# Kernel tuning notes

Measured on AMD Instinct MI355X. Metric: run time of the kernel, lower is better.

The kernel has to match this reference:

```python
import jax, jax.numpy as jnp
import numpy as np

EMB = 3          # embedding_size
NSIG = 1         # n_sigma
FG_W = 1.0       # foreground_weight
W_INST, W_VAR, W_SEED = 1.0, 10.0, 1.0
K_MAX = 8        # fixed number of instance ids (1..K_MAX); 0 is background


def _xyzm(T, H, W):
    # buffer is linspace over the FULL grid (32,800,2000), then sliced
    t = jnp.linspace(0.0, 0.1, 32)[:T]
    y = jnp.linspace(0.0, 1.6, 800)[:H]
    x = jnp.linspace(0.0, 4.16, 2000)[:W]
    tt = jnp.broadcast_to(t[:, None, None], (T, H, W))
    yy = jnp.broadcast_to(y[None, :, None], (T, H, W))
    xx = jnp.broadcast_to(x[None, None, :], (T, H, W))
    return jnp.stack([tt, yy, xx], 0)  # [3,T,H,W]


def _lovasz_hinge_flat(logits, labels):
    # standard Berman lovasz hinge on flat [N] logits/labels (labels in {0,1})
    signs = 2.0 * labels - 1.0
    errors = 1.0 - logits * signs
    order = jnp.argsort(-errors)             # descending errors
    errors_sorted = errors[order]
    gt_sorted = labels[order]
    gts = gt_sorted.sum()
    inter = gts - jnp.cumsum(gt_sorted)
    union = gts + jnp.cumsum(1.0 - gt_sorted)
    jac = 1.0 - inter / union
    grad = jnp.concatenate([jac[:1], jac[1:] - jac[:-1]])
    return jnp.dot(jax.nn.relu(errors_sorted), jax.lax.stop_gradient(grad))


def _forward(prediction, instances):
    B, C, T, H, W = prediction.shape
    xyzm = _xyzm(T, H, W).astype(prediction.dtype)

    emb = jnp.tanh(prediction[:, :EMB])                 # [B,3,T,H,W]
    spatial = emb + xyzm[None]                          # spatial_emb
    sigma = prediction[:, EMB]                          # [B,T,H,W] (n_sigma=1)
    seed = jax.nn.sigmoid(prediction[:, EMB + NSIG])    # [B,T,H,W]

    ids = jnp.arange(1, K_MAX + 1)
    masks = (instances[:, None] == ids[None, :, None, None, None]).astype(prediction.dtype)  # [B,K,T,H,W]
    counts = masks.sum((2, 3, 4))                       # [B,K]
    present = (counts > 0).astype(prediction.dtype)
    safe = jnp.maximum(counts, 1.0)

    # per-instance center of xyzm (to_center=True) and mean sigma
    centers = jnp.einsum('cthw,bkthw->bkc', xyzm, masks) / safe[..., None]   # [B,K,3]
    s_mean = jnp.einsum('bthw,bkthw->bk', sigma, masks) / safe               # [B,K]
    s_sg = jax.lax.stop_gradient(s_mean)

    # var loss: mean over mask of (sigma - stop_grad(s_mean))^2
    sig2 = jnp.einsum('bthw,bkthw->bk', sigma * sigma, masks) / safe
    var_k = sig2 - 2.0 * s_sg * s_mean + s_sg * s_sg                          # [B,K]

    # gaussian distance map: exp(-s * ||spatial - center||^2)
    s_exp = jnp.exp(s_mean * 10.0)                                            # [B,K]
    e2 = jnp.sum(spatial * spatial, axis=1)                                   # [B,T,H,W]
    ec = jnp.einsum('bcthw,bkc->bkthw', spatial, centers)                     # [B,K,T,H,W]
    c2 = jnp.sum(centers * centers, axis=-1)                                  # [B,K]
    sqdist = e2[:, None] - 2.0 * ec + c2[:, :, None, None, None]
    dist = jnp.exp(-s_exp[:, :, None, None, None] * sqdist)                   # [B,K,T,H,W]

    # lovasz hinge per instance
    logits = (dist * 2.0 - 1.0).reshape(B * K_MAX, -1)
    labels_flat = masks.reshape(B * K_MAX, -1)
    inst_k = jax.vmap(_lovasz_hinge_flat)(logits, labels_flat).reshape(B, K_MAX)

    obj = present.sum(1)
    safe_obj = jnp.maximum(obj, 1.0)
    inst_loss = (inst_k * present).sum(1) / safe_obj
    var_loss = (var_k * present).sum(1) / safe_obj

    # seed loss: background -> 0, foreground -> stop_grad(dist)
    bg = (instances == 0).astype(prediction.dtype)
    seed_bg = jnp.sum(bg * seed * seed, axis=(1, 2, 3))
    dsg = jax.lax.stop_gradient(dist)
    seed_fg = FG_W * jnp.sum(masks * (seed[:, None] - dsg) ** 2, axis=(1, 2, 3, 4))
    seed_loss = (seed_bg + seed_fg) / (H * W)

    return jnp.mean(W_INST * inst_loss + W_VAR * var_loss + W_SEED * seed_loss)


def setup_inputs() -> dict:
    key = jax.random.key(0)
    k1, k2, k3 = jax.random.split(key, 3)
    prediction = jax.random.normal(k1, (2, 5, 8, 256, 512), dtype=jnp.float32)
    instances = jax.random.randint(k2, (2, 8, 256, 512), 0, 9, dtype=jnp.int32)
    labels = jax.random.randint(k3, (2, 8, 256, 512), 0, 2, dtype=jnp.int32)
    return {"prediction": prediction, "instances": instances, "labels": labels}


def reference(prediction, instances, labels):
    # `labels` is accepted by the torch forward but unused in the loss math
    return _forward(prediction, instances)
```

## Files before the change

### kernel.cpp

```cpp
#include <hip/hip_runtime.h>
#include <math.h>

#define BB 2
#define KK 8
#define NB 256
#define HALF_NB_F 128.0f
#define FAR_CUT 5.5452f

#define PXB_H 1024
#define GRID_H 2048
#define PXB_A 4096
#define GRID_A 512
#define NPART_A 256

#define STEP_T (0.1f/31.0f)
#define STEP_Y (1.6f/799.0f)
#define STEP_X (4.16f/1999.0f)

#define OFF_ACC 0
#define OFF_PRM 100
#define OFF_GH2 512
#define OFF_PARTA 9216
#define OFF_SEED2 34816
#define OFF_HIST_F 40960

__global__ __launch_bounds__(256) void k_acc(const float* __restrict__ pred,
                                             const int* __restrict__ inst,
                                             float* __restrict__ ws) {
  int tid = threadIdx.x, blk = blockIdx.x;
  int b = blk >> 8;
  int rbase = (blk & 255) * PXB_A;
  const float* sig_p = pred + ((size_t)b * 5 << 20) + (3 << 20);
  const int* ip = inst + ((size_t)b << 20);
  float acc[48];
  #pragma unroll
  for (int f = 0; f < 48; ++f) acc[f] = 0.f;
  for (int it = 0; it < 4; ++it) {
    int r = rbase + it * 1024 + 4 * tid;
    float4 sg4 = *(const float4*)(sig_p + r);
    int4 id4 = *(const int4*)(ip + r);
    float tf = (float)(r >> 17), hf = (float)((r >> 9) & 255), wf = (float)(r & 511);
    float sv[4] = {sg4.x, sg4.y, sg4.z, sg4.w};
    int iv[4] = {id4.x, id4.y, id4.z, id4.w};
    #pragma unroll
    for (int j = 0; j < 4; ++j) {
      #pragma unroll
      for (int k = 0; k < KK; ++k) {
        float m = (iv[j] == k + 1) ? 1.f : 0.f;
        acc[k*6+0] += m;
        acc[k*6+1] += m * sv[j];
        acc[k*6+2] += m * sv[j] * sv[j];
        acc[k*6+3] += m * tf;
        acc[k*6+4] += m * hf;
        acc[k*6+5] += m * (wf + (float)j);
      }
    }
  }
  __shared__ float lds[4 * 48];
  int lane = tid & 63, wv = tid >> 6;
  #pragma unroll
  for (int f = 0; f < 48; ++f) {
    float v = acc[f];
    for (int o = 32; o; o >>= 1) v += __shfl_down(v, o);
    if (lane == 0) lds[wv * 48 + f] = v;
  }
  __syncthreads();
  if (tid < 48)
    ws[OFF_PARTA + ((size_t)b * 48 + tid) * NPART_A + (blk & 255)]
      = lds[tid] + lds[48 + tid] + lds[96 + tid] + lds[144 + tid];
}

__global__ __launch_bounds__(256) void k_params(float* __restrict__ ws) {
  __shared__ float accs[96];
  int tid = threadIdx.x;
  if (tid < 96) {
    const float* p = ws + OFF_PARTA + (size_t)tid * NPART_A;
    float s0 = 0.f, s1 = 0.f, s2 = 0.f, s3 = 0.f;
    for (int j = 0; j < NPART_A; j += 4) {
      s0 += p[j]; s1 += p[j+1]; s2 += p[j+2]; s3 += p[j+3];
    }
    accs[tid] = (s0 + s1) + (s2 + s3);
  }
  __syncthreads();
  if (tid < 16) {
    float* a = &accs[(tid >> 3) * 48 + (tid & 7) * 6];
    float cnt = a[0], s1 = a[1], s2 = a[2], st = a[3], sy = a[4], sx = a[5];
    float safe = fmaxf(cnt, 1.f);
    float smean = s1 / safe;
    ws[OFF_ACC + tid*6 + 0] = cnt;
    ws[OFF_PRM + tid*6 + 0] = st * STEP_T / safe;
    ws[OFF_PRM + tid*6 + 1] = sy * STEP_Y / safe;
    ws[OFF_PRM + tid*6 + 2] = sx * STEP_X / safe;
    ws[OFF_PRM + tid*6 + 3] = __expf(10.f * smean);
    ws[OFF_PRM + tid*6 + 4] = s2 / safe - smean * smean;
    ws[OFF_PRM + tid*6 + 5] = (cnt > 0.f) ? 1.f : 0.f;
  }
}

__device__ __forceinline__ float fast_tanh(float x) {
  x = fminf(fmaxf(x, -15.f), 15.f);
  float ex = __expf(2.f * x);
  return (ex - 1.f) / (ex + 1.f);
}

__global__ __launch_bounds__(256, 8) void k_hist(const float* __restrict__ pred,
                                                 const int* __restrict__ inst,
                                                 float* __restrict__ ws) {
  __shared__ unsigned int hist[KK * NB];
  __shared__ float Ps[KK * 4];
  __shared__ unsigned int pmask_s;
  __shared__ float wred[8];
  int tid = threadIdx.x;
  int blk = blockIdx.x;
  int b = blk >> 10;
  for (int i = tid; i < KK * NB; i += 256) hist[i] = 0u;
  if (tid < KK) {
    int seg = b * 8 + tid;
    Ps[tid*4+0] = ws[OFF_PRM + seg*6 + 0];
    Ps[tid*4+1] = ws[OFF_PRM + seg*6 + 1];
    Ps[tid*4+2] = ws[OFF_PRM + seg*6 + 2];
    Ps[tid*4+3] = ws[OFF_PRM + seg*6 + 3];
  }
  if (tid == 0) {
    unsigned m = 0;
    for (int k = 0; k < KK; ++k)
      if (ws[OFF_PRM + (b*8+k)*6 + 5] > 0.f) m |= 1u << k;
    pmask_s = m;
  }
  __syncthreads();
  unsigned pmask = pmask_s;
  int r = (blk & 1023) * PXB_H + 4 * tid;
  const float* pb = pred + ((size_t)b * 5 << 20);
  float tf = (float)(r >> 17), hf = (float)((r >> 9) & 255);
  int w = r & 511;
  float4 p0 = *(const float4*)(pb + r);
  float4 p1 = *(const float4*)(pb + (1 << 20) + r);
  float4 p2 = *(const float4*)(pb + (2 << 20) + r);
  float4 p4 = *(const float4*)(pb + (4 << 20) + r);
  int4 id4 = *(const int4*)(inst + ((size_t)b << 20) + r);
  int iv[4] = {id4.x, id4.y, id4.z, id4.w};
  float e0[4], e1[4], e2[4], sd[4];
  {
    float q0[4] = {p0.x,p0.y,p0.z,p0.w}, q1[4] = {p1.x,p1.y,p1.z,p1.w};
    float q2[4] = {p2.x,p2.y,p2.z,p2.w}, q4[4] = {p4.x,p4.y,p4.z,p4.w};
    #pragma unroll
    for (int j = 0; j < 4; ++j) {
      e0[j] = fast_tanh(q0[j]) + tf * STEP_T;
      e1[j] = fast_tanh(q1[j]) + hf * STEP_Y;
      e2[j] = fast_tanh(q2[j]) + (float)(w + j) * STEP_X;
      sd[j] = 1.f / (1.f + __expf(-q4[j]));
    }
  }
  float sbg = 0.f, sfg = 0.f;
  #pragma unroll
  for (int j = 0; j < 4; ++j) if (iv[j] == 0) sbg += sd[j] * sd[j];
  int lane = tid & 63;
  #pragma unroll
  for (int k = 0; k < KK; ++k) {
    if (!((pmask >> k) & 1)) continue;
    float4 P = *(float4*)&Ps[k * 4];
    float ssq[4];
    bool lab[4], any_need = false;
    #pragma unroll
    for (int j = 0; j < 4; ++j) {
      float dt = e0[j] - P.x, dy = e1[j] - P.y, dx = e2[j] - P.z;
      ssq[j] = P.w * (dt*dt + dy*dy + dx*dx);
      lab[j] = (iv[j] == k + 1);
      any_need |= (ssq[j] < FAR_CUT) | lab[j];
    }
    if (__any(any_need)) {
      unsigned long long mlo[4], mto[4], mla[4];
      int bin[4]; bool low[4], top[4];
      #pragma unroll
      for (int j = 0; j < 4; ++j) {
        float d = __expf(-ssq[j]);
        if (lab[j]) { float df = sd[j] - d; sfg += df * df; }
        float e = lab[j] ? (2.f - 2.f * d) : (2.f * d);
        bin[j] = min((int)(e * HALF_NB_F), NB - 1);
        low[j] = (bin[j] == 0); top[j] = (bin[j] == NB - 1);
        mla[j] = __ballot(lab[j]); mlo[j] = __ballot(low[j]); mto[j] = __ballot(top[j]);
      }
      if (lane == 0) {
        unsigned vlow = 0, vtop = 0;
        #pragma unroll
        for (int j = 0; j < 4; ++j) {
          vlow += (unsigned)__popcll(mlo[j] & ~mla[j]) + ((unsigned)__popcll(mlo[j] & mla[j]) << 16);
          vtop += (unsigned)__popcll(mto[j] & ~mla[j]) + ((unsigned)__popcll(mto[j] & mla[j]) << 16);
        }
        if (vlow) atomicAdd(&hist[k * NB], vlow);
        if (vtop) atomicAdd(&hist[k * NB + NB - 1], vtop);
      }
      #pragma unroll
      for (int j = 0; j < 4; ++j)
        if (!low[j] && !top[j]) atomicAdd(&hist[k * NB + bin[j]], lab[j] ? 0x10000u : 1u);
    } else {
      if (lane == 0) atomicAdd(&hist[k * NB], 256u);
    }
  }
  for (int off = 32; off; off >>= 1) {
    sbg += __shfl_down(sbg, off);
    sfg += __shfl_down(sfg, off);
  }
  if (lane == 0) { wred[(tid >> 6) * 2] = sbg; wred[(tid >> 6) * 2 + 1] = sfg; }
  __syncthreads();
  if (tid == 0)
    ((float2*)(ws + OFF_SEED2))[blk] =
      make_float2(wred[0] + wred[2] + wred[4] + wred[6],
                  wred[1] + wred[3] + wred[5] + wred[7]);
  uint4* gp = (uint4*)((unsigned int*)(ws + OFF_HIST_F) + (size_t)blk * (KK * NB));
  const uint4* hs = (const uint4*)hist;
  #pragma unroll
  for (int i = 0; i < 2; ++i) gp[i * 256 + tid] = hs[i * 256 + tid];
}

__global__ __launch_bounds__(256) void k_red(float* __restrict__ ws) {
  int blk = blockIdx.x;
  int tid = threadIdx.x;
  int seg = blk >> 4, range = blk & 15;
  int b = seg >> 3, k = seg & 7;
  __shared__ unsigned long long sred[256];
  int bin_off = tid & 15;
  int pgrp = tid >> 4;
  const unsigned int* gh = (const unsigned int*)(ws + OFF_HIST_F);
  size_t base = ((size_t)b * 1024 + (size_t)pgrp * 64) * (KK * NB)
              + (size_t)k * NB + (size_t)range * 16 + bin_off;
  unsigned int neg = 0, pos = 0;
  #pragma unroll 4
  for (int j = 0; j < 64; ++j) {
    unsigned v = gh[base + (size_t)j * (KK * NB)];
    neg += v & 0xFFFFu; pos += v >> 16;
  }
  sred[tid] = ((unsigned long long)pos << 32) | neg;
  __syncthreads();
  if (tid < 16) {
    unsigned long long a = 0;
    #pragma unroll
    for (int j = 0; j < 16; ++j) a += sred[tid + j * 16];
    ((unsigned long long*)(ws + OFF_GH2))[seg * NB + range * 16 + tid] = a;
  }
}

__global__ __launch_bounds__(256) void k_fin(float* __restrict__ ws, float* __restrict__ out) {
  int tid = threadIdx.x;
  int lane = tid & 63, wv = tid >> 6;
  __shared__ double segtot[16];
  __shared__ float sdb[4], sdf[4];
  {
    const float2* sp = (const float2*)(ws + OFF_SEED2);
    float sb = 0.f, sf = 0.f;
    #pragma unroll
    for (int j = 0; j < 8; ++j) { float2 v = sp[tid * 8 + j]; sb += v.x; sf += v.y; }
    for (int o = 32; o; o >>= 1) { sb += __shfl_down(sb, o); sf += __shfl_down(sf, o); }
    if (lane == 0) { sdb[wv] = sb; sdf[wv] = sf; }
  }
  const unsigned long long* gh2 = (const unsigned long long*)(ws + OFF_GH2);
  for (int s = wv; s < 16; s += 4) {
    double total = 0.0;
    if (ws[OFF_PRM + s*6 + 5] != 0.f) {
      double gts = (double)ws[OFF_ACC + s*6 + 0];
      unsigned long long carry = 0;
      double sum = 0.0;
      for (int c = 0; c < NB / 64; ++c) {
        int bin = NB - 1 - (c * 64 + lane);
        unsigned long long v = gh2[s * NB + bin];
        unsigned long long orig = v;
        #pragma unroll
        for (int o = 1; o < 64; o <<= 1) {
          unsigned long long u = (unsigned long long)__shfl_up((long long)v, o, 64);
          if (lane >= o) v += u;
        }
        v += carry;
        if (orig) {
          unsigned int ip = (unsigned)(v >> 32), in_ = (unsigned)v;
          unsigned int ppx = (unsigned)(orig >> 32), nnx = (unsigned)orig;
          double ep = (double)(ip - ppx), en = (double)(in_ - nnx);
          double js = 1.0 - (gts - ep) / (gts + en);
          double je = 1.0 - (gts - (double)ip) / (gts + (double)in_);
          sum += ((double)bin + 0.5) * (2.0 / NB) * (je - js);
        }
        carry = (unsigned long long)__shfl((long long)v, 63, 64);
      }
      for (int o = 32; o; o >>= 1) sum += __shfl_down(sum, o);
      total = sum;
    }
    if (lane == 0) segtot[s] = total;
  }
  __syncthreads();
  if (tid == 0) {
    double tot = 0.0;
    for (int bb = 0; bb < BB; ++bb) {
      double il = 0.0, vl = 0.0, ob = 0.0;
      for (int k2 = 0; k2 < KK; ++k2) {
        int s2 = bb * 8 + k2;
        double pr = (double)ws[OFF_PRM + s2*6 + 5];
        il += segtot[s2] * pr;
        vl += (double)ws[OFF_PRM + s2*6 + 4] * pr;
        ob += pr;
      }
      double so = (ob > 1.0) ? ob : 1.0;
      double sbg = (double)sdb[bb * 2] + (double)sdb[bb * 2 + 1];
      double sfg = (double)sdf[bb * 2] + (double)sdf[bb * 2 + 1];
      tot += il / so + 10.0 * vl / so + (sbg + sfg) / (256.0 * 512.0);
    }
    out[0] = (float)(tot / BB);
  }
}

extern "C" void kernel_launch(void* const* d_in, const int* in_sizes, int n_in,
                              void* d_out, int out_size, void* d_ws, size_t ws_size,
                              hipStream_t stream) {
  const float* pred = (const float*)d_in[0];
  const int* inst = (const int*)d_in[1];
  float* ws = (float*)d_ws;
  float* out = (float*)d_out;
  k_acc<<<GRID_A, 256, 0, stream>>>(pred, inst, ws);
  k_params<<<1, 256, 0, stream>>>(ws);
  k_hist<<<GRID_H, 256, 0, stream>>>(pred, inst, ws);
  k_red<<<256, 256, 0, stream>>>(ws);
  k_fin<<<1, 256, 0, stream>>>(ws, out);
}
```

Before: 145.3 us.

## Expand distance quadratic, simplify histogram binning, retile kernels, use nontemporal loads

Precomputes per-instance coefficients so the scaled squared distance becomes a few FMAs on a per-pixel norm, instead of a subtraction and square per axis. Drops the wave-level any-check and the low/top ballot aggregation. Each pixel now either counts toward a per-wave skip counter or does its own LDS atomic. Also halves k_acc work per block, doubles k_hist block size to 512 threads, halves the partial-histogram count, and switches streaming loads to nontemporal. Per-pixel atomics on the top bin may contend more than the old ballot path.

Result: no change. 146.2 us (+0.6%).

```diff
diff --git a/kernel.cpp b/kernel.cpp
--- a/kernel.cpp
+++ b/kernel.cpp
@@ -5,40 +5,53 @@
 #define KK 8
 #define NB 256
 #define HALF_NB_F 128.0f
-#define FAR_CUT 5.5452f
-
-#define PXB_H 1024
-#define GRID_H 2048
-#define PXB_A 4096
-#define GRID_A 512
-#define NPART_A 256
+#define FAR_CUT 5.545177444479562f
+
+#define PXB_H 2048
+#define GRID_H 1024
+#define PXB_A 2048
+#define GRID_A 1024
+#define NPART_A 512
 
 #define STEP_T (0.1f/31.0f)
 #define STEP_Y (1.6f/799.0f)
 #define STEP_X (4.16f/1999.0f)
 
-#define OFF_ACC 0
-#define OFF_PRM 100
+#define OFF_CNT 0
+#define OFF_PRM 32
 #define OFF_GH2 512
 #define OFF_PARTA 9216
-#define OFF_SEED2 34816
-#define OFF_HIST_F 40960
+#define OFF_SEED2 59392
+#define OFF_HIST_F 65536
+
+typedef float nvf4 __attribute__((ext_vector_type(4)));
+typedef int   nvi4 __attribute__((ext_vector_type(4)));
+
+__device__ __forceinline__ float4 ntload4f(const float* p) {
+  nvf4 v = __builtin_nontemporal_load((const nvf4*)p);
+  return make_float4(v.x, v.y, v.z, v.w);
+}
+__device__ __forceinline__ int4 ntload4i(const int* p) {
+  nvi4 v = __builtin_nontemporal_load((const nvi4*)p);
+  return make_int4(v.x, v.y, v.z, v.w);
+}
 
 __global__ __launch_bounds__(256) void k_acc(const float* __restrict__ pred,
                                              const int* __restrict__ inst,
                                              float* __restrict__ ws) {
   int tid = threadIdx.x, blk = blockIdx.x;
-  int b = blk >> 8;
-  int rbase = (blk & 255) * PXB_A;
+  int b = blk >> 9;
+  int rbase = (blk & 511) * PXB_A;
   const float* sig_p = pred + ((size_t)b * 5 << 20) + (3 << 20);
   const int* ip = inst + ((size_t)b << 20);
   float acc[48];
   #pragma unroll
   for (int f = 0; f < 48; ++f) acc[f] = 0.f;
-  for (int it = 0; it < 4; ++it) {
+  #pragma unroll
+  for (int it = 0; it < 2; ++it) {
     int r = rbase + it * 1024 + 4 * tid;
-    float4 sg4 = *(const float4*)(sig_p + r);
-    int4 id4 = *(const int4*)(ip + r);
+    float4 sg4 = ntload4f(sig_p + r);
+    int4 id4 = ntload4i(ip + r);
     float tf = (float)(r >> 17), hf = (float)((r >> 9) & 255), wf = (float)(r & 511);
     float sv[4] = {sg4.x, sg4.y, sg4.z, sg4.w};
     int iv[4] = {id4.x, id4.y, id4.z, id4.w};
@@ -66,7 +79,7 @@
   }
   __syncthreads();
   if (tid < 48)
-    ws[OFF_PARTA + ((size_t)b * 48 + tid) * NPART_A + (blk & 255)]
+    ws[OFF_PARTA + ((size_t)b * 48 + tid) * NPART_A + (blk & 511)]
       = lds[tid] + lds[48 + tid] + lds[96 + tid] + lds[144 + tid];
 }
 
@@ -87,13 +100,19 @@
     float cnt = a[0], s1 = a[1], s2 = a[2], st = a[3], sy = a[4], sx = a[5];
     float safe = fmaxf(cnt, 1.f);
     float smean = s1 / safe;
-    ws[OFF_ACC + tid*6 + 0] = cnt;
-    ws[OFF_PRM + tid*6 + 0] = st * STEP_T / safe;
-    ws[OFF_PRM + tid*6 + 1] = sy * STEP_Y / safe;
-    ws[OFF_PRM + tid*6 + 2] = sx * STEP_X / safe;
-    ws[OFF_PRM + tid*6 + 3] = __expf(10.f * smean);
-    ws[OFF_PRM + tid*6 + 4] = s2 / safe - smean * smean;
-    ws[OFF_PRM + tid*6 + 5] = (cnt > 0.f) ? 1.f : 0.f;
+    float A = __expf(10.f * smean);
+    float ct = st * STEP_T / safe;
+    float cy = sy * STEP_Y / safe;
+    float cx = sx * STEP_X / safe;
+    ws[OFF_CNT + tid] = cnt;
+    ws[OFF_PRM + tid*8 + 0] = 2.f * A * ct;
+    ws[OFF_PRM + tid*8 + 1] = 2.f * A * cy;
+    ws[OFF_PRM + tid*8 + 2] = 2.f * A * cx;
+    ws[OFF_PRM + tid*8 + 3] = A;
+    ws[OFF_PRM + tid*8 + 4] = A * (ct*ct + cy*cy + cx*cx);
+    ws[OFF_PRM + tid*8 + 5] = s2 / safe - smean * smean;
+    ws[OFF_PRM + tid*8 + 6] = (cnt > 0.f) ? 1.f : 0.f;
+    ws[OFF_PRM + tid*8 + 7] = 0.f;
   }
 }
 
@@ -103,43 +122,32 @@
   return (ex - 1.f) / (ex + 1.f);
 }
 
-__global__ __launch_bounds__(256, 8) void k_hist(const float* __restrict__ pred,
+__global__ __launch_bounds__(512, 8) void k_hist(const float* __restrict__ pred,
                                                  const int* __restrict__ inst,
                                                  float* __restrict__ ws) {
   __shared__ unsigned int hist[KK * NB];
-  __shared__ float Ps[KK * 4];
-  __shared__ unsigned int pmask_s;
-  __shared__ float wred[8];
+  __shared__ float Ps[KK * 8];
+  __shared__ float wred[16];
   int tid = threadIdx.x;
   int blk = blockIdx.x;
-  int b = blk >> 10;
-  for (int i = tid; i < KK * NB; i += 256) hist[i] = 0u;
-  if (tid < KK) {
-    int seg = b * 8 + tid;
-    Ps[tid*4+0] = ws[OFF_PRM + seg*6 + 0];
-    Ps[tid*4+1] = ws[OFF_PRM + seg*6 + 1];
-    Ps[tid*4+2] = ws[OFF_PRM + seg*6 + 2];
-    Ps[tid*4+3] = ws[OFF_PRM + seg*6 + 3];
-  }
-  if (tid == 0) {
-    unsigned m = 0;
-    for (int k = 0; k < KK; ++k)
-      if (ws[OFF_PRM + (b*8+k)*6 + 5] > 0.f) m |= 1u << k;
-    pmask_s = m;
-  }
-  __syncthreads();
-  unsigned pmask = pmask_s;
-  int r = (blk & 1023) * PXB_H + 4 * tid;
+  int b = blk >> 9;
+  for (int i = tid; i < KK * NB; i += 512) hist[i] = 0u;
+  if (tid < KK * 8) Ps[tid] = ws[OFF_PRM + b * 64 + tid];
+  __syncthreads();
+  unsigned pmask = 0;
+  #pragma unroll
+  for (int k = 0; k < KK; ++k) if (Ps[k*8 + 6] > 0.f) pmask |= 1u << k;
+  int r = (blk & 511) * PXB_H + 4 * tid;
   const float* pb = pred + ((size_t)b * 5 << 20);
   float tf = (float)(r >> 17), hf = (float)((r >> 9) & 255);
   int w = r & 511;
-  float4 p0 = *(const float4*)(pb + r);
-  float4 p1 = *(const float4*)(pb + (1 << 20) + r);
-  float4 p2 = *(const float4*)(pb + (2 << 20) + r);
-  float4 p4 = *(const float4*)(pb + (4 << 20) + r);
-  int4 id4 = *(const int4*)(inst + ((size_t)b << 20) + r);
+  float4 p0 = ntload4f(pb + r);
+  float4 p1 = ntload4f(pb + (1 << 20) + r);
+  float4 p2 = ntload4f(pb + (2 << 20) + r);
+  float4 p4 = ntload4f(pb + (4 << 20) + r);
+  int4 id4 = ntload4i(inst + ((size_t)b << 20) + r);
   int iv[4] = {id4.x, id4.y, id4.z, id4.w};
-  float e0[4], e1[4], e2[4], sd[4];
+  float e0[4], e1[4], e2[4], ee[4], sd[4];
   {
     float q0[4] = {p0.x,p0.y,p0.z,p0.w}, q1[4] = {p1.x,p1.y,p1.z,p1.w};
     float q2[4] = {p2.x,p2.y,p2.z,p2.w}, q4[4] = {p4.x,p4.y,p4.z,p4.w};
@@ -148,6 +156,7 @@
       e0[j] = fast_tanh(q0[j]) + tf * STEP_T;
       e1[j] = fast_tanh(q1[j]) + hf * STEP_Y;
       e2[j] = fast_tanh(q2[j]) + (float)(w + j) * STEP_X;
+      ee[j] = e0[j]*e0[j] + e1[j]*e1[j] + e2[j]*e2[j];
       sd[j] = 1.f / (1.f + __expf(-q4[j]));
     }
   }
@@ -155,47 +164,33 @@
   #pragma unroll
   for (int j = 0; j < 4; ++j) if (iv[j] == 0) sbg += sd[j] * sd[j];
   int lane = tid & 63;
+  unsigned hot[KK];
+  #pragma unroll
+  for (int k = 0; k < KK; ++k) hot[k] = 0u;
   #pragma unroll
   for (int k = 0; k < KK; ++k) {
     if (!((pmask >> k) & 1)) continue;
-    float4 P = *(float4*)&Ps[k * 4];
-    float ssq[4];
-    bool lab[4], any_need = false;
+    float Bt = Ps[k*8+0], By = Ps[k*8+1], Bx = Ps[k*8+2], A = Ps[k*8+3], C = Ps[k*8+4];
     #pragma unroll
     for (int j = 0; j < 4; ++j) {
-      float dt = e0[j] - P.x, dy = e1[j] - P.y, dx = e2[j] - P.z;
-      ssq[j] = P.w * (dt*dt + dy*dy + dx*dx);
-      lab[j] = (iv[j] == k + 1);
-      any_need |= (ssq[j] < FAR_CUT) | lab[j];
-    }
-    if (__any(any_need)) {
-      unsigned long long mlo[4], mto[4], mla[4];
-      int bin[4]; bool low[4], top[4];
-      #pragma unroll
-      for (int j = 0; j < 4; ++j) {
-        float d = __expf(-ssq[j]);
-        if (lab[j]) { float df = sd[j] - d; sfg += df * df; }
-        float e = lab[j] ? (2.f - 2.f * d) : (2.f * d);
-        bin[j] = min((int)(e * HALF_NB_F), NB - 1);
-        low[j] = (bin[j] == 0); top[j] = (bin[j] == NB - 1);
-        mla[j] = __ballot(lab[j]); mlo[j] = __ballot(low[j]); mto[j] = __ballot(top[j]);
+      float ssq = fmaf(-Bt, e0[j], fmaf(-By, e1[j], fmaf(-Bx, e2[j], fmaf(A, ee[j], C))));
+      bool lab = (iv[j] == k + 1);
+      bool skip = (ssq >= FAR_CUT) && !lab;
+      unsigned long long ms = __ballot(skip);
+      hot[k] += (unsigned)__popcll(ms);
+      if (!skip) {
+        float d = __expf(-ssq);
+        if (lab) { float df = sd[j] - d; sfg += df * df; }
+        float e = lab ? (2.f - 2.f * d) : (2.f * d);
+        int bin = min((int)(e * HALF_NB_F), NB - 1);
+        atomicAdd(&hist[k * NB + bin], lab ? 0x10000u : 1u);
       }
-      if (lane == 0) {
-        unsigned vlow = 0, vtop = 0;
-        #pragma unroll
-        for (int j = 0; j < 4; ++j) {
-          vlow += (unsigned)__popcll(mlo[j] & ~mla[j]) + ((unsigned)__popcll(mlo[j] & mla[j]) << 16);
-          vtop += (unsigned)__popcll(mto[j] & ~mla[j]) + ((unsigned)__popcll(mto[j] & mla[j]) << 16);
-        }
-        if (vlow) atomicAdd(&hist[k * NB], vlow);
-        if (vtop) atomicAdd(&hist[k * NB + NB - 1], vtop);
-      }
-      #pragma unroll
-      for (int j = 0; j < 4; ++j)
-        if (!low[j] && !top[j]) atomicAdd(&hist[k * NB + bin[j]], lab[j] ? 0x10000u : 1u);
-    } else {
-      if (lane == 0) atomicAdd(&hist[k * NB], 256u);
-    }
+    }
+  }
+  if (lane == 0) {
+    #pragma unroll
+    for (int k = 0; k < KK; ++k)
+      if (hot[k]) atomicAdd(&hist[k * NB], hot[k]);
   }
   for (int off = 32; off; off >>= 1) {
     sbg += __shfl_down(sbg, off);
@@ -203,14 +198,14 @@
   }
   if (lane == 0) { wred[(tid >> 6) * 2] = sbg; wred[(tid >> 6) * 2 + 1] = sfg; }
   __syncthreads();
-  if (tid == 0)
-    ((float2*)(ws + OFF_SEED2))[blk] =
-      make_float2(wred[0] + wred[2] + wred[4] + wred[6],
-                  wred[1] + wred[3] + wred[5] + wred[7]);
+  if (tid == 0) {
+    float b0 = 0.f, f0 = 0.f;
+    #pragma unroll
+    for (int v = 0; v < 8; ++v) { b0 += wred[v*2]; f0 += wred[v*2+1]; }
+    ((float2*)(ws + OFF_SEED2))[blk] = make_float2(b0, f0);
+  }
   uint4* gp = (uint4*)((unsigned int*)(ws + OFF_HIST_F) + (size_t)blk * (KK * NB));
-  const uint4* hs = (const uint4*)hist;
-  #pragma unroll
-  for (int i = 0; i < 2; ++i) gp[i * 256 + tid] = hs[i * 256 + tid];
+  gp[tid] = ((const uint4*)hist)[tid];
 }
 
 __global__ __launch_bounds__(256) void k_red(float* __restrict__ ws) {
@@ -222,11 +217,11 @@
   int bin_off = tid & 15;
   int pgrp = tid >> 4;
   const unsigned int* gh = (const unsigned int*)(ws + OFF_HIST_F);
-  size_t base = ((size_t)b * 1024 + (size_t)pgrp * 64) * (KK * NB)
+  size_t base = ((size_t)b * 512 + (size_t)pgrp * 32) * (KK * NB)
               + (size_t)k * NB + (size_t)range * 16 + bin_off;
   unsigned int neg = 0, pos = 0;
   #pragma unroll 4
-  for (int j = 0; j < 64; ++j) {
+  for (int j = 0; j < 32; ++j) {
     unsigned v = gh[base + (size_t)j * (KK * NB)];
     neg += v & 0xFFFFu; pos += v >> 16;
   }
@@ -249,15 +244,15 @@
     const float2* sp = (const float2*)(ws + OFF_SEED2);
     float sb = 0.f, sf = 0.f;
     #pragma unroll
-    for (int j = 0; j < 8; ++j) { float2 v = sp[tid * 8 + j]; sb += v.x; sf += v.y; }
+    for (int j = 0; j < 4; ++j) { float2 v = sp[tid * 4 + j]; sb += v.x; sf += v.y; }
     for (int o = 32; o; o >>= 1) { sb += __shfl_down(sb, o); sf += __shfl_down(sf, o); }
     if (lane == 0) { sdb[wv] = sb; sdf[wv] = sf; }
   }
   const unsigned long long* gh2 = (const unsigned long long*)(ws + OFF_GH2);
   for (int s = wv; s < 16; s += 4) {
     double total = 0.0;
-    if (ws[OFF_PRM + s*6 + 5] != 0.f) {
-      double gts = (double)ws[OFF_ACC + s*6 + 0];
+    if (ws[OFF_PRM + s*8 + 6] != 0.f) {
+      double gts = (double)ws[OFF_CNT + s];
       unsigned long long carry = 0;
       double sum = 0.0;
       for (int c = 0; c < NB / 64; ++c) {
@@ -292,9 +287,9 @@
       double il = 0.0, vl = 0.0, ob = 0.0;
       for (int k2 = 0; k2 < KK; ++k2) {
         int s2 = bb * 8 + k2;
-        double pr = (double)ws[OFF_PRM + s2*6 + 5];
+        double pr = (double)ws[OFF_PRM + s2*8 + 6];
         il += segtot[s2] * pr;
-        vl += (double)ws[OFF_PRM + s2*6 + 4] * pr;
+        vl += (double)ws[OFF_PRM + s2*8 + 5] * pr;
         ob += pr;
       }
       double so = (ob > 1.0) ? ob : 1.0;
@@ -315,7 +310,7 @@
   float* out = (float*)d_out;
   k_acc<<<GRID_A, 256, 0, stream>>>(pred, inst, ws);
   k_params<<<1, 256, 0, stream>>>(ws);
-  k_hist<<<GRID_H, 256, 0, stream>>>(pred, inst, ws);
+  k_hist<<<GRID_H, 512, 0, stream>>>(pred, inst, ws);
   k_red<<<256, 256, 0, stream>>>(ws);
   k_fin<<<1, 256, 0, stream>>>(ws, out);
 }
```
